# Kernel tuning notes

Hardware: AMD Instinct MI355X
Metric: run time of the kernel (lower is better)

## Reference

```python
import jax, jax.numpy as jnp
import numpy as np

B, S, D_IN, D_H, D_OUT, NB = 4, 4096, 1024, 1024, 1024, 8
BD = D_H // NB  # block size of the block-diagonal gate projections
R_MIN, R_MAX, EPS = 0.9, 0.999, 1e-8


def setup_inputs() -> dict:
    key = jax.random.key(0)
    ks = jax.random.split(key, 8)
    x = jax.random.normal(ks[0], (B, S, D_IN), dtype=jnp.float32)
    h0 = jnp.zeros((B, D_H), dtype=jnp.float32)
    # input projection Dense(d_hidden)
    W_in = jax.random.normal(ks[1], (D_IN, D_H), dtype=jnp.float32) / np.sqrt(D_IN)
    b_in = jnp.zeros((D_H,), dtype=jnp.float32)
    # two BlockDiagonalLinear gate projections (n_blocks blocks of [BD, BD])
    Wgx = jax.random.normal(ks[2], (NB, BD, BD), dtype=jnp.float32) / np.sqrt(BD)
    bgx = jnp.zeros((D_H,), dtype=jnp.float32)
    Wga = jax.random.normal(ks[3], (NB, BD, BD), dtype=jnp.float32) / np.sqrt(BD)
    bga = jnp.zeros((D_H,), dtype=jnp.float32)
    # stable_init_real: softplus(param) == -log(r) with r ~ U[r_min, r_max] in magnitude
    u = jax.random.uniform(ks[4], (D_H,), dtype=jnp.float32)
    a_real = 0.5 * jnp.log(u * (R_MAX**2 - R_MIN**2) + R_MIN**2 + EPS)
    a_real_param = jnp.log(jnp.exp(-a_real) - 1.0)
    # output projection Dense(d_out)
    W_out = jax.random.normal(ks[5], (D_H, D_OUT), dtype=jnp.float32) / np.sqrt(D_H)
    b_out = jnp.zeros((D_OUT,), dtype=jnp.float32)
    return dict(x=x, h0=h0, W_in=W_in, b_in=b_in, Wgx=Wgx, bgx=bgx,
                Wga=Wga, bga=bga, a_real_param=a_real_param,
                W_out=W_out, b_out=b_out)


def _block_diag_linear(x, W, b):
    # x: [B,S,D_H] -> split into NB blocks of BD, per-block matmul
    xb = x.reshape(x.shape[0], x.shape[1], NB, BD)
    y = jnp.einsum('bsni,nio->bsno', xb, W)
    return y.reshape(x.shape[0], x.shape[1], D_H) + b


def reference(x, h0, W_in, b_in, Wgx, bgx, Wga, bga, a_real_param, W_out, b_out):
    # input projection
    x = x @ W_in + b_in  # [B,S,D_H]
    # input-dependent gates (sigmoid of block-diagonal projections)
    gate_x = jax.nn.sigmoid(_block_diag_linear(x, Wgx, bgx))
    gate_a = jax.nn.sigmoid(_block_diag_linear(x, Wga, bga))
    # real-only RG-LRU recurrence coefficient: a = exp(-8 * gate_a * softplus(c))
    log_a = -8.0 * gate_a * jax.nn.softplus(a_real_param)  # [B,S,D_H], <= 0
    a = jnp.exp(log_a)
    # gated input with sqrt(1 - a^2) normalization (sqrt_bound_derivative fwd == sqrt)
    gx = gate_x * x * jnp.sqrt(1.0 - jnp.exp(2.0 * log_a))
    # fold initial state into the first step: h_1 = a_1 * h0 + gx_1
    gx = gx.at[:, 0].add(a[:, 0] * h0)
    # linear scan h_t = a_t * h_{t-1} + gx_t via associative scan over seq axis
    def combine(c1, c2):
        a1, x1 = c1
        a2, x2 = c2
        return (a2 * a1, a2 * x1 + x2)
    _, h = jax.lax.associative_scan(combine, (a, gx), axis=1)  # [B,S,D_H]
    out = h @ W_out + b_out  # [B,S,D_OUT]
    return out, h[:, -1]
```

## Files before the change

kernel.cpp:

```cpp
#include <hip/hip_runtime.h>

#define B_SZ 4
#define SEQ 4096
#define DIN 1024
#define DH 1024
#define DOUT 1024
#define NBLK 8
#define MTOK (B_SZ * SEQ)
#define CHUNK 64
#define NCHUNK (SEQ / CHUNK)

typedef _Float16 half8 __attribute__((ext_vector_type(8)));
typedef _Float16 half4v __attribute__((ext_vector_type(4)));
typedef float f32x4 __attribute__((ext_vector_type(4)));

__device__ __forceinline__ void gl_lds16(const void* g, void* l) {
  __builtin_amdgcn_global_load_lds((__attribute__((address_space(1))) void*)g,
                                   (__attribute__((address_space(3))) void*)l,
                                   16, 0, 0);
}

__global__ __launch_bounds__(256)
void prep_kernel(const float* __restrict__ x, _Float16* __restrict__ x_h,
                 const float* __restrict__ Win, const float* __restrict__ Wout,
                 const float* __restrict__ Wgx, const float* __restrict__ Wga,
                 _Float16* __restrict__ WinT, _Float16* __restrict__ WoutT,
                 _Float16* __restrict__ WgxT, _Float16* __restrict__ WgaT) {
  __shared__ float tile[64][65];
  if (blockIdx.x < 16384) {
    const int gid = blockIdx.x * 256 + threadIdx.x;
    const float4 v = ((const float4*)x)[gid];
    half4v h;
    h[0] = (_Float16)v.x; h[1] = (_Float16)v.y; h[2] = (_Float16)v.z; h[3] = (_Float16)v.w;
    ((half4v*)x_h)[gid] = h;
    return;
  }
  int t = blockIdx.x - 16384;
  const float* src; _Float16* dst; int C; size_t bo = 0;
  if (t < 256)      { src = Win;  dst = WinT;  C = 1024; }
  else if (t < 512) { src = Wout; dst = WoutT; C = 1024; t -= 256; }
  else if (t < 544) { int u = t - 512; src = Wgx; dst = WgxT; C = 128;
                      bo = (size_t)(u >> 2) * (128 * 128); t = u & 3; }
  else              { int u = t - 544; src = Wga; dst = WgaT; C = 128;
                      bo = (size_t)(u >> 2) * (128 * 128); t = u & 3; }
  const int nbx = C >> 6;
  const int r0 = (t / nbx) * 64, c0 = (t % nbx) * 64;
  const int tr = threadIdx.x >> 6, tc = threadIdx.x & 63;
#pragma unroll
  for (int i = 0; i < 64; i += 4)
    tile[tr + i][tc] = src[bo + (size_t)(r0 + tr + i) * C + c0 + tc];
  __syncthreads();
#pragma unroll
  for (int i = 0; i < 64; i += 4) {
    const int cc = i + tr;
    dst[bo + (size_t)(c0 + cc) * C + r0 + tc] = (_Float16)tile[tc][cc];
  }
}

template <int OUT_F32>
__global__ __launch_bounds__(256)
void gemm_bt(const _Float16* __restrict__ A, const _Float16* __restrict__ Bt,
             const float* __restrict__ bias, void* __restrict__ C,
             int M, int N, int K) {
  __shared__ __align__(16) _Float16 As[128 * 64];
  __shared__ __align__(16) _Float16 Bs[128 * 64];
  const int tid = threadIdx.x;
  const int wave = tid >> 6, lane = tid & 63;
  const int m0 = blockIdx.x * 128, n0 = blockIdx.y * 128;
  const int wm = (wave >> 1) * 64, wn = (wave & 1) * 64;
  const int row = lane & 15, quad = lane >> 4;
  const int srow = lane >> 3, scol = (lane & 7) * 8;

  f32x4 acc[4][4] = {};
  for (int kt = 0; kt < K; kt += 64) {
#pragma unroll
    for (int ci = 0; ci < 4; ci++) {
      const int c = wave * 4 + ci;
      gl_lds16(A  + (size_t)(m0 + c * 8 + srow) * K + kt + scol, As + c * 512);
      gl_lds16(Bt + (size_t)(n0 + c * 8 + srow) * K + kt + scol, Bs + c * 512);
    }
    __syncthreads();
#pragma unroll
    for (int kk = 0; kk < 64; kk += 32) {
      half8 af[4], bf[4];
#pragma unroll
      for (int i = 0; i < 4; i++)
        af[i] = *(const half8*)&As[(wm + i * 16 + row) * 64 + kk + quad * 8];
#pragma unroll
      for (int i = 0; i < 4; i++)
        bf[i] = *(const half8*)&Bs[(wn + i * 16 + row) * 64 + kk + quad * 8];
#pragma unroll
      for (int i = 0; i < 4; i++)
#pragma unroll
        for (int j = 0; j < 4; j++)
          acc[i][j] = __builtin_amdgcn_mfma_f32_16x16x32_f16(af[i], bf[j], acc[i][j], 0, 0, 0);
    }
    __syncthreads();
  }
  float bv[4];
#pragma unroll
  for (int j = 0; j < 4; j++) bv[j] = bias[n0 + wn + j * 16 + row];
#pragma unroll
  for (int i = 0; i < 4; i++) {
#pragma unroll
    for (int r = 0; r < 4; r++) {
      const int m = m0 + wm + i * 16 + quad * 4 + r;
      const size_t base = (size_t)m * N + n0 + wn + row;
#pragma unroll
      for (int j = 0; j < 4; j++) {
        const float v = acc[i][j][r] + bv[j];
        if (OUT_F32) ((float*)C)[base + j * 16] = v;
        else         ((_Float16*)C)[base + j * 16] = (_Float16)v;
      }
    }
  }
}

__global__ __launch_bounds__(256)
void gates_v3(const _Float16* __restrict__ xp,
              const _Float16* __restrict__ WxT, const _Float16* __restrict__ WaT,
              const float* __restrict__ bgx, const float* __restrict__ bga,
              const float* __restrict__ arp,
              _Float16* __restrict__ a_out, _Float16* __restrict__ gx_out,
              float* __restrict__ cA, float* __restrict__ cH) {
  const int tid = threadIdx.x;
  const int wave = tid >> 6, lane = tid & 63;
  const int m0 = blockIdx.x * 128, nb = blockIdx.y;
  const int wm = (wave >> 1) * 64, wn = (wave & 1) * 64;
  const int row = lane & 15, quad = lane >> 4;
  const _Float16* WxB = WxT + (size_t)nb * (128 * 128);
  const _Float16* WaB = WaT + (size_t)nb * (128 * 128);
  const _Float16* xb = xp + (size_t)m0 * DH + nb * 128;

  f32x4 accx[4][4] = {}, acca[4][4] = {};
#pragma unroll
  for (int kk = 0; kk < 128; kk += 32) {
    half8 af[4];
#pragma unroll
    for (int i = 0; i < 4; i++)
      af[i] = *(const half8*)&xb[(size_t)(wm + i * 16 + row) * DH + kk + quad * 8];
#pragma unroll
    for (int j = 0; j < 4; j++) {
      const size_t wo = (size_t)(wn + j * 16 + row) * 128 + kk + quad * 8;
      const half8 bx = *(const half8*)&WxB[wo];
      const half8 ba = *(const half8*)&WaB[wo];
#pragma unroll
      for (int i = 0; i < 4; i++) {
        accx[i][j] = __builtin_amdgcn_mfma_f32_16x16x32_f16(af[i], bx, accx[i][j], 0, 0, 0);
        acca[i][j] = __builtin_amdgcn_mfma_f32_16x16x32_f16(af[i], ba, acca[i][j], 0, 0, 0);
      }
    }
  }

  const int b_idx = (m0 + wm) >> 12;
  const int c_idx = ((m0 + wm) & (SEQ - 1)) >> 6;
  float bxv[4], bav[4], cd[4];
#pragma unroll
  for (int j = 0; j < 4; j++) {
    const int d = nb * 128 + wn + j * 16 + row;
    bxv[j] = bgx[d]; bav[j] = bga[d];
    cd[j] = log1pf(expf(arp[d]));
  }
  float Arun[4], Hrun[4];
#pragma unroll
  for (int j = 0; j < 4; j++) { Arun[j] = 1.f; Hrun[j] = 0.f; }

#pragma unroll
  for (int i = 0; i < 4; i++) {
    float Aseg[4], Hseg[4];
#pragma unroll
    for (int j = 0; j < 4; j++) { Aseg[j] = 1.f; Hseg[j] = 0.f; }
#pragma unroll
    for (int r = 0; r < 4; r++) {
      const int tl = wm + i * 16 + quad * 4 + r;
      const size_t rowbase = (size_t)(m0 + tl) * DH + nb * 128 + wn + row;
      _Float16 ah[4], gh[4];
#pragma unroll
      for (int j = 0; j < 4; j++) {
        const float px = accx[i][j][r] + bxv[j];
        const float pa = acca[i][j][r] + bav[j];
        const float sx = 1.f / (1.f + __expf(-px));
        const float sa = 1.f / (1.f + __expf(-pa));
        const float a = __expf(-8.f * sa * cd[j]);
        const float n2 = fmaxf(1.f - a * a, 0.f);
        const float xv = (float)xb[(size_t)tl * DH + wn + j * 16 + row];
        ah[j] = (_Float16)a;
        gh[j] = (_Float16)(sx * xv * sqrtf(n2));
        const float ar = (float)ah[j], gr = (float)gh[j];
        Aseg[j] *= ar;
        Hseg[j] = fmaf(ar, Hseg[j], gr);
      }
#pragma unroll
      for (int j = 0; j < 4; j++) a_out[rowbase + j * 16] = ah[j];
#pragma unroll
      for (int j = 0; j < 4; j++) gx_out[rowbase + j * 16] = gh[j];
    }
#pragma unroll
    for (int j = 0; j < 4; j++) {
      float A1 = Aseg[j], H1 = Hseg[j];
      float A2 = __shfl_down(A1, 16, 64), H2 = __shfl_down(H1, 16, 64);
      H1 = fmaf(A2, H1, H2); A1 *= A2;
      A2 = __shfl_down(A1, 32, 64); H2 = __shfl_down(H1, 32, 64);
      H1 = fmaf(A2, H1, H2); A1 *= A2;
      Hrun[j] = fmaf(A1, Hrun[j], H1);
      Arun[j] *= A1;
    }
  }
  if (lane < 16) {
    const int base = c_idx * (B_SZ * DH) + b_idx * DH + nb * 128 + wn + lane;
#pragma unroll
    for (int j = 0; j < 4; j++) {
      cA[base + j * 16] = Arun[j];
      cH[base + j * 16] = Hrun[j];
    }
  }
}

__global__ __launch_bounds__(256)
void scan_p2(const float* __restrict__ cA, const float* __restrict__ cH,
             const float* __restrict__ h0, float* __restrict__ cin,
             float* __restrict__ hlast) {
  const int wave = threadIdx.x >> 6, lane = threadIdx.x & 63;
  const int g = blockIdx.x * 4 + wave;
  float A = cA[(size_t)lane * (B_SZ * DH) + g], H = cH[(size_t)lane * (B_SZ * DH) + g];
#pragma unroll
  for (int d = 1; d < 64; d <<= 1) {
    const float Ap = __shfl_up(A, d, 64), Hp = __shfl_up(H, d, 64);
    if (lane >= d) { H = fmaf(A, Hp, H); A *= Ap; }
  }
  const float h0g = h0[g];
  if (lane == 63) hlast[g] = fmaf(A, h0g, H);
  float Ae = __shfl_up(A, 1, 64), He = __shfl_up(H, 1, 64);
  if (lane == 0) { Ae = 1.f; He = 0.f; }
  cin[(size_t)lane * (B_SZ * DH) + g] = fmaf(Ae, h0g, He);
}

__global__ __launch_bounds__(256)
void scan_p3(const _Float16* __restrict__ a, const _Float16* __restrict__ gx,
             const float* __restrict__ cin, _Float16* __restrict__ h) {
  const int gtid = blockIdx.x * 256 + threadIdx.x;
  const int d = gtid & (DH - 1);
  const int bc = gtid >> 10;
  const int b = bc >> 6, c = bc & (NCHUNK - 1);
  const size_t base = ((size_t)(b * SEQ + c * CHUNK)) * DH + d;
  float carry = cin[c * (B_SZ * DH) + b * DH + d];
#pragma unroll 4
  for (int i = 0; i < CHUNK; i++) {
    const float av = (float)a[base + (size_t)i * DH];
    const float gv = (float)gx[base + (size_t)i * DH];
    carry = fmaf(av, carry, gv);
    h[base + (size_t)i * DH] = (_Float16)carry;
  }
}

extern "C" void kernel_launch(void* const* d_in, const int* in_sizes, int n_in,
                              void* d_out, int out_size, void* d_ws, size_t ws_size,
                              hipStream_t stream) {
  const float* x     = (const float*)d_in[0];
  const float* h0    = (const float*)d_in[1];
  const float* W_in  = (const float*)d_in[2];
  const float* b_in  = (const float*)d_in[3];
  const float* Wgx   = (const float*)d_in[4];
  const float* bgx   = (const float*)d_in[5];
  const float* Wga   = (const float*)d_in[6];
  const float* bga   = (const float*)d_in[7];
  const float* arp   = (const float*)d_in[8];
  const float* W_out = (const float*)d_in[9];
  const float* b_out = (const float*)d_in[10];
  float* out = (float*)d_out;
  float* hlast = out + (size_t)MTOK * DOUT;

  char* p = (char*)d_ws;
  auto take = [&](size_t bytes) { char* r = p; p += (bytes + 255) & ~(size_t)255; return r; };
  _Float16* x_h   = (_Float16*)take((size_t)MTOK * DIN * 2);
  _Float16* xp    = (_Float16*)take((size_t)MTOK * DH * 2);
  _Float16* a_buf = (_Float16*)take((size_t)MTOK * DH * 2);
  _Float16* gxb   = (_Float16*)take((size_t)MTOK * DH * 2);
  _Float16* WinT  = (_Float16*)take((size_t)DIN * DH * 2);
  _Float16* WoutT = (_Float16*)take((size_t)DH * DOUT * 2);
  _Float16* WgxT  = (_Float16*)take((size_t)NBLK * 128 * 128 * 2);
  _Float16* WgaT  = (_Float16*)take((size_t)NBLK * 128 * 128 * 2);
  float* cA   = (float*)take((size_t)NCHUNK * B_SZ * DH * 4);
  float* cH   = (float*)take((size_t)NCHUNK * B_SZ * DH * 4);
  float* cin  = (float*)take((size_t)NCHUNK * B_SZ * DH * 4);
  _Float16* h_buf = x_h;

  prep_kernel<<<16384 + 576, 256, 0, stream>>>(x, x_h, W_in, W_out, Wgx, Wga,
                                               WinT, WoutT, WgxT, WgaT);
  gemm_bt<0><<<dim3(MTOK / 128, DH / 128), 256, 0, stream>>>(x_h, WinT, b_in, xp, MTOK, DH, DIN);
  gates_v3<<<dim3(MTOK / 128, NBLK), 256, 0, stream>>>(
      xp, WgxT, WgaT, bgx, bga, arp, a_buf, gxb, cA, cH);
  scan_p2<<<(B_SZ * DH) / 4, 256, 0, stream>>>(cA, cH, h0, cin, hlast);
  scan_p3<<<(B_SZ * NCHUNK * DH) / 256, 256, 0, stream>>>(a_buf, gxb, cin, h_buf);
  gemm_bt<1><<<dim3(MTOK / 128, DOUT / 128), 256, 0, stream>>>(h_buf, WoutT, b_out, out, MTOK, DOUT, DH);
}
```

Baseline: 364.5 us.

## Fuse input projection GEMM with block-diagonal gate computation

Merges the input-projection GEMM and the gate kernel into one kernel. Each 128x128 output tile of x@W_in is kept in swizzled LDS and consumed directly by the block-diagonal gate matmuls, the recurrence-coefficient math and the chunk scan. This removes the xp round trip through global memory and one kernel launch. The gate phase is split into two halves to limit register pressure. The cost is an un-pipelined GEMM main loop (load, sync, compute) and higher register and LDS use per block.

```diff
diff --git a/kernel.cpp b/kernel.cpp
--- a/kernel.cpp
+++ b/kernel.cpp
@@ -18,6 +18,10 @@
   __builtin_amdgcn_global_load_lds((__attribute__((address_space(1))) void*)g,
                                    (__attribute__((address_space(3))) void*)l,
                                    16, 0, 0);
+}
+
+__device__ __forceinline__ int swz_h(int r, int c) {
+  return (((r << 8) | (c << 1)) ^ ((r & 7) << 4)) >> 1;
 }
 
 __global__ __launch_bounds__(256)
@@ -117,101 +121,146 @@
 }
 
 __global__ __launch_bounds__(256)
-void gates_v3(const _Float16* __restrict__ xp,
-              const _Float16* __restrict__ WxT, const _Float16* __restrict__ WaT,
-              const float* __restrict__ bgx, const float* __restrict__ bga,
-              const float* __restrict__ arp,
-              _Float16* __restrict__ a_out, _Float16* __restrict__ gx_out,
-              float* __restrict__ cA, float* __restrict__ cH) {
+void gemm1_gates(const _Float16* __restrict__ A, const _Float16* __restrict__ Bt,
+                 const float* __restrict__ bias,
+                 const _Float16* __restrict__ WxT, const _Float16* __restrict__ WaT,
+                 const float* __restrict__ bgx, const float* __restrict__ bga,
+                 const float* __restrict__ arp,
+                 _Float16* __restrict__ a_out, _Float16* __restrict__ gx_out,
+                 float* __restrict__ cA, float* __restrict__ cH) {
+  __shared__ __align__(16) _Float16 smem[128 * 128];
+  _Float16* const As = smem;
+  _Float16* const Bs = smem + 128 * 64;
   const int tid = threadIdx.x;
   const int wave = tid >> 6, lane = tid & 63;
-  const int m0 = blockIdx.x * 128, nb = blockIdx.y;
+  const int m0 = blockIdx.x * 128, nb = blockIdx.y, n0 = nb * 128;
   const int wm = (wave >> 1) * 64, wn = (wave & 1) * 64;
   const int row = lane & 15, quad = lane >> 4;
-  const _Float16* WxB = WxT + (size_t)nb * (128 * 128);
-  const _Float16* WaB = WaT + (size_t)nb * (128 * 128);
-  const _Float16* xb = xp + (size_t)m0 * DH + nb * 128;
-
-  f32x4 accx[4][4] = {}, acca[4][4] = {};
-#pragma unroll
-  for (int kk = 0; kk < 128; kk += 32) {
-    half8 af[4];
+  const int srow = lane >> 3, scol = (lane & 7) * 8;
+
+  f32x4 acc[4][4] = {};
+  for (int kt = 0; kt < DIN; kt += 64) {
+#pragma unroll
+    for (int ci = 0; ci < 4; ci++) {
+      const int c = wave * 4 + ci;
+      gl_lds16(A  + (size_t)(m0 + c * 8 + srow) * DIN + kt + scol, As + c * 512);
+      gl_lds16(Bt + (size_t)(n0 + c * 8 + srow) * DIN + kt + scol, Bs + c * 512);
+    }
+    __syncthreads();
+#pragma unroll
+    for (int kk = 0; kk < 64; kk += 32) {
+      half8 af[4], bf[4];
+#pragma unroll
+      for (int i = 0; i < 4; i++)
+        af[i] = *(const half8*)&As[(wm + i * 16 + row) * 64 + kk + quad * 8];
+#pragma unroll
+      for (int i = 0; i < 4; i++)
+        bf[i] = *(const half8*)&Bs[(wn + i * 16 + row) * 64 + kk + quad * 8];
+#pragma unroll
+      for (int i = 0; i < 4; i++)
+#pragma unroll
+        for (int j = 0; j < 4; j++)
+          acc[i][j] = __builtin_amdgcn_mfma_f32_16x16x32_f16(af[i], bf[j], acc[i][j], 0, 0, 0);
+    }
+    __syncthreads();
+  }
+
+  {
+    float bv[4];
+#pragma unroll
+    for (int j = 0; j < 4; j++) bv[j] = bias[n0 + wn + j * 16 + row];
 #pragma unroll
     for (int i = 0; i < 4; i++)
-      af[i] = *(const half8*)&xb[(size_t)(wm + i * 16 + row) * DH + kk + quad * 8];
-#pragma unroll
-    for (int j = 0; j < 4; j++) {
-      const size_t wo = (size_t)(wn + j * 16 + row) * 128 + kk + quad * 8;
-      const half8 bx = *(const half8*)&WxB[wo];
-      const half8 ba = *(const half8*)&WaB[wo];
-#pragma unroll
-      for (int i = 0; i < 4; i++) {
-        accx[i][j] = __builtin_amdgcn_mfma_f32_16x16x32_f16(af[i], bx, accx[i][j], 0, 0, 0);
-        acca[i][j] = __builtin_amdgcn_mfma_f32_16x16x32_f16(af[i], ba, acca[i][j], 0, 0, 0);
-      }
-    }
-  }
-
+#pragma unroll
+      for (int r = 0; r < 4; r++) {
+        const int tl = wm + i * 16 + quad * 4 + r;
+#pragma unroll
+        for (int j = 0; j < 4; j++)
+          smem[swz_h(tl, wn + j * 16 + row)] = (_Float16)(acc[i][j][r] + bv[j]);
+      }
+  }
+  __syncthreads();
+
+  const _Float16* const WxB = WxT + (size_t)nb * (128 * 128);
+  const _Float16* const WaB = WaT + (size_t)nb * (128 * 128);
   const int b_idx = (m0 + wm) >> 12;
   const int c_idx = ((m0 + wm) & (SEQ - 1)) >> 6;
-  float bxv[4], bav[4], cd[4];
-#pragma unroll
-  for (int j = 0; j < 4; j++) {
-    const int d = nb * 128 + wn + j * 16 + row;
-    bxv[j] = bgx[d]; bav[j] = bga[d];
-    cd[j] = log1pf(expf(arp[d]));
-  }
-  float Arun[4], Hrun[4];
-#pragma unroll
-  for (int j = 0; j < 4; j++) { Arun[j] = 1.f; Hrun[j] = 0.f; }
-
-#pragma unroll
-  for (int i = 0; i < 4; i++) {
-    float Aseg[4], Hseg[4];
-#pragma unroll
-    for (int j = 0; j < 4; j++) { Aseg[j] = 1.f; Hseg[j] = 0.f; }
-#pragma unroll
-    for (int r = 0; r < 4; r++) {
-      const int tl = wm + i * 16 + quad * 4 + r;
-      const size_t rowbase = (size_t)(m0 + tl) * DH + nb * 128 + wn + row;
-      _Float16 ah[4], gh[4];
-#pragma unroll
-      for (int j = 0; j < 4; j++) {
-        const float px = accx[i][j][r] + bxv[j];
-        const float pa = acca[i][j][r] + bav[j];
-        const float sx = 1.f / (1.f + __expf(-px));
-        const float sa = 1.f / (1.f + __expf(-pa));
-        const float a = __expf(-8.f * sa * cd[j]);
-        const float n2 = fmaxf(1.f - a * a, 0.f);
-        const float xv = (float)xb[(size_t)tl * DH + wn + j * 16 + row];
-        ah[j] = (_Float16)a;
-        gh[j] = (_Float16)(sx * xv * sqrtf(n2));
-        const float ar = (float)ah[j], gr = (float)gh[j];
-        Aseg[j] *= ar;
-        Hseg[j] = fmaf(ar, Hseg[j], gr);
-      }
-#pragma unroll
-      for (int j = 0; j < 4; j++) a_out[rowbase + j * 16] = ah[j];
-#pragma unroll
-      for (int j = 0; j < 4; j++) gx_out[rowbase + j * 16] = gh[j];
-    }
-#pragma unroll
-    for (int j = 0; j < 4; j++) {
-      float A1 = Aseg[j], H1 = Hseg[j];
-      float A2 = __shfl_down(A1, 16, 64), H2 = __shfl_down(H1, 16, 64);
-      H1 = fmaf(A2, H1, H2); A1 *= A2;
-      A2 = __shfl_down(A1, 32, 64); H2 = __shfl_down(H1, 32, 64);
-      H1 = fmaf(A2, H1, H2); A1 *= A2;
-      Hrun[j] = fmaf(A1, Hrun[j], H1);
-      Arun[j] *= A1;
-    }
-  }
-  if (lane < 16) {
-    const int base = c_idx * (B_SZ * DH) + b_idx * DH + nb * 128 + wn + lane;
-#pragma unroll
-    for (int j = 0; j < 4; j++) {
-      cA[base + j * 16] = Arun[j];
-      cH[base + j * 16] = Hrun[j];
+  const int cbase = c_idx * (B_SZ * DH) + b_idx * DH + n0 + wn + row;
+
+#pragma unroll 1
+  for (int jp = 0; jp < 2; jp++) {
+    f32x4 accx[4][2] = {}, acca[4][2] = {};
+#pragma unroll
+    for (int kk = 0; kk < 128; kk += 32) {
+      half8 af[4];
+#pragma unroll
+      for (int i = 0; i < 4; i++)
+        af[i] = *(const half8*)&smem[swz_h(wm + i * 16 + row, kk + quad * 8)];
+#pragma unroll
+      for (int jj = 0; jj < 2; jj++) {
+        const size_t wo = (size_t)(wn + (jp * 2 + jj) * 16 + row) * 128 + kk + quad * 8;
+        const half8 bx = *(const half8*)&WxB[wo];
+        const half8 ba = *(const half8*)&WaB[wo];
+#pragma unroll
+        for (int i = 0; i < 4; i++) {
+          accx[i][jj] = __builtin_amdgcn_mfma_f32_16x16x32_f16(af[i], bx, accx[i][jj], 0, 0, 0);
+          acca[i][jj] = __builtin_amdgcn_mfma_f32_16x16x32_f16(af[i], ba, acca[i][jj], 0, 0, 0);
+        }
+      }
+    }
+    float bxv[2], bav[2], cd[2];
+#pragma unroll
+    for (int jj = 0; jj < 2; jj++) {
+      const int d = n0 + wn + (jp * 2 + jj) * 16 + row;
+      bxv[jj] = bgx[d]; bav[jj] = bga[d];
+      cd[jj] = log1pf(expf(arp[d]));
+    }
+    float Arun[2] = {1.f, 1.f}, Hrun[2] = {0.f, 0.f};
+#pragma unroll
+    for (int i = 0; i < 4; i++) {
+      float Aseg[2] = {1.f, 1.f}, Hseg[2] = {0.f, 0.f};
+#pragma unroll
+      for (int r = 0; r < 4; r++) {
+        const int tl = wm + i * 16 + quad * 4 + r;
+        const size_t rowbase = (size_t)(m0 + tl) * DH + n0 + wn + row;
+        _Float16 ah[2], gh[2];
+#pragma unroll
+        for (int jj = 0; jj < 2; jj++) {
+          const float px = accx[i][jj][r] + bxv[jj];
+          const float pa = acca[i][jj][r] + bav[jj];
+          const float sx = 1.f / (1.f + __expf(-px));
+          const float sa = 1.f / (1.f + __expf(-pa));
+          const float a = __expf(-8.f * sa * cd[jj]);
+          const float n2 = fmaxf(1.f - a * a, 0.f);
+          const float xv = (float)smem[swz_h(tl, wn + (jp * 2 + jj) * 16 + row)];
+          ah[jj] = (_Float16)a;
+          gh[jj] = (_Float16)(sx * xv * sqrtf(n2));
+          const float ar = (float)ah[jj], gr = (float)gh[jj];
+          Aseg[jj] *= ar;
+          Hseg[jj] = fmaf(ar, Hseg[jj], gr);
+        }
+#pragma unroll
+        for (int jj = 0; jj < 2; jj++) a_out[rowbase + (jp * 2 + jj) * 16] = ah[jj];
+#pragma unroll
+        for (int jj = 0; jj < 2; jj++) gx_out[rowbase + (jp * 2 + jj) * 16] = gh[jj];
+      }
+#pragma unroll
+      for (int jj = 0; jj < 2; jj++) {
+        float A1 = Aseg[jj], H1 = Hseg[jj];
+        float A2 = __shfl_down(A1, 16, 64), H2 = __shfl_down(H1, 16, 64);
+        H1 = fmaf(A2, H1, H2); A1 *= A2;
+        A2 = __shfl_down(A1, 32, 64); H2 = __shfl_down(H1, 32, 64);
+        H1 = fmaf(A2, H1, H2); A1 *= A2;
+        Hrun[jj] = fmaf(A1, Hrun[jj], H1);
+        Arun[jj] *= A1;
+      }
+    }
+    if (lane < 16) {
+#pragma unroll
+      for (int jj = 0; jj < 2; jj++) {
+        cA[cbase + (jp * 2 + jj) * 16] = Arun[jj];
+        cH[cbase + (jp * 2 + jj) * 16] = Hrun[jj];
+      }
     }
   }
 }
@@ -273,7 +322,6 @@
   char* p = (char*)d_ws;
   auto take = [&](size_t bytes) { char* r = p; p += (bytes + 255) & ~(size_t)255; return r; };
   _Float16* x_h   = (_Float16*)take((size_t)MTOK * DIN * 2);
-  _Float16* xp    = (_Float16*)take((size_t)MTOK * DH * 2);
   _Float16* a_buf = (_Float16*)take((size_t)MTOK * DH * 2);
   _Float16* gxb   = (_Float16*)take((size_t)MTOK * DH * 2);
   _Float16* WinT  = (_Float16*)take((size_t)DIN * DH * 2);
@@ -287,9 +335,8 @@
 
   prep_kernel<<<16384 + 576, 256, 0, stream>>>(x, x_h, W_in, W_out, Wgx, Wga,
                                                WinT, WoutT, WgxT, WgaT);
-  gemm_bt<0><<<dim3(MTOK / 128, DH / 128), 256, 0, stream>>>(x_h, WinT, b_in, xp, MTOK, DH, DIN);
-  gates_v3<<<dim3(MTOK / 128, NBLK), 256, 0, stream>>>(
-      xp, WgxT, WgaT, bgx, bga, arp, a_buf, gxb, cA, cH);
+  gemm1_gates<<<dim3(MTOK / 128, NBLK), 256, 0, stream>>>(
+      x_h, WinT, b_in, WgxT, WgaT, bgx, bga, arp, a_buf, gxb, cA, cH);
   scan_p2<<<(B_SZ * DH) / 4, 256, 0, stream>>>(cA, cH, h0, cin, hlast);
   scan_p3<<<(B_SZ * NCHUNK * DH) / 256, 256, 0, stream>>>(a_buf, gxb, cin, h_buf);
   gemm_bt<1><<<dim3(MTOK / 128, DOUT / 128), 256, 0, stream>>>(h_buf, WoutT, b_out, out, MTOK, DOUT, DH);
```

After: 374.9 us. +2.8%, slower.
